# Performance work log

Measured on AMD Instinct MI355X. Metric: run time of the kernel, lower is better.

The kernel has to match this reference:

```python
import jax, jax.numpy as jnp
import numpy as np

B, N, D, J, L = 8, 2046, 128, 128, 2  # batch, ops, feature len, jobs, blocks
C = N + 2  # ops + appended begin/end rows


def setup_inputs() -> dict:
    key = jax.random.key(0)
    ks = jax.random.split(key, 40)

    def w(k, shape, fan_in):
        return jax.random.normal(k, shape, jnp.float32) / np.float32(np.sqrt(fan_in))

    inp = {}
    inp["operation_features"] = jax.random.normal(ks[0], (B, N, D), jnp.float32)
    inp["same_type_mask"] = (jax.random.uniform(ks[1], (B, N, N)) > 0.5).astype(jnp.float32)
    inp["relations"] = jax.random.randint(ks[2], (B, N, 2), 0, N, jnp.int32)
    inp["begins_idx"] = jax.random.randint(ks[3], (B, J), 0, N, jnp.int32)
    inp["ends_idx"] = jax.random.randint(ks[4], (B, J), 0, N, jnp.int32)
    # begin_end_init params
    inp["init_bp_w"] = w(ks[5], (D, D), D); inp["init_bp_b"] = jnp.zeros((D,), jnp.float32)
    inp["init_ep_w"] = w(ks[6], (D, D), D); inp["init_ep_b"] = jnp.zeros((D,), jnp.float32)
    # per-block params, stacked on leading L axis
    inp["be_bp_w"] = w(ks[7], (L, D, D), D); inp["be_bp_b"] = jnp.zeros((L, D), jnp.float32)
    inp["be_ep_w"] = w(ks[8], (L, D, D), D); inp["be_ep_b"] = jnp.zeros((L, D), jnp.float32)
    inp["seq_mix_w"] = w(ks[9], (L, 3 * D, D), 3 * D); inp["seq_mix_b"] = jnp.zeros((L, D), jnp.float32)
    inp["attn_w_w"] = w(ks[10], (L, D, 3 * D), D); inp["attn_w_b"] = jnp.zeros((L, 3 * D), jnp.float32)
    inp["score_w"] = w(ks[11], (L, 2 * D), 2 * D); inp["score_b"] = jnp.zeros((L,), jnp.float32)
    inp["attn_out_w"] = w(ks[12], (L, D, D), D); inp["attn_out_b"] = jnp.zeros((L, D), jnp.float32)
    inp["mix_w"] = w(ks[13], (L, 2 * D, D), 2 * D); inp["mix_b"] = jnp.zeros((L, D), jnp.float32)
    return inp


def _begin_end(ops, begins_idx, ends_idx, bp_w, bp_b, ep_w, ep_b):
    gb = jnp.take_along_axis(ops, begins_idx[..., None], axis=1)  # [B,J,D]
    ge = jnp.take_along_axis(ops, ends_idx[..., None], axis=1)
    begin = jnp.mean(gb @ bp_w + bp_b, axis=1)  # [B,D]
    end = jnp.mean(ge @ ep_w + ep_b, axis=1)
    return begin, end


def _forward(operation_features, same_type_mask,
             init_bp_w, init_bp_b, init_ep_w, init_ep_b,
             be_bp_w, be_bp_b, be_ep_w, be_ep_b,
             seq_mix_w, seq_mix_b, attn_w_w, attn_w_b,
             score_w, score_b, attn_out_w, attn_out_b,
             mix_w, mix_b, relations, begins_idx, ends_idx):
    begin, end = _begin_end(operation_features, begins_idx, ends_idx,
                            init_bp_w, init_bp_b, init_ep_w, init_ep_b)
    feats = jnp.concatenate([operation_features, begin[:, None], end[:, None]], axis=1)  # [B,C,D]
    # -1 sentinels point to appended begin/end rows
    rel_p = jnp.where(relations[..., 0] == -1, N, relations[..., 0])  # [B,N]
    rel_s = jnp.where(relations[..., 1] == -1, N + 1, relations[..., 1])
    mask = jnp.zeros((B, C, C), jnp.float32)
    mask = mask.at[:, :N, :N].set(same_type_mask)
    mask = mask.at[:, N, N].set(1.0).at[:, N + 1, N + 1].set(1.0)

    for l in range(L):
        # --- OperationTimeRelationEncoder ---
        pred = jnp.take_along_axis(feats, rel_p[..., None], axis=1)  # [B,N,D]
        succ = jnp.take_along_axis(feats, rel_s[..., None], axis=1)
        mixed = jnp.concatenate([feats[:, :N], pred, succ], axis=-1) @ seq_mix_w[l] + seq_mix_b[l]
        b2, e2 = _begin_end(feats, begins_idx, ends_idx,
                            be_bp_w[l], be_bp_b[l], be_ep_w[l], be_ep_b[l])
        seq_feats = jnp.concatenate([mixed, b2[:, None], e2[:, None]], axis=1)  # [B,C,D]
        # --- SelfAttention (GAT-style concat score) ---
        qkv = feats @ attn_w_w[l] + attn_w_b[l]
        q, k, v = jnp.split(qkv, 3, axis=-1)  # each [B,C,D]
        wq, wk = score_w[l][:D], score_w[l][D:]
        # score(concat(q_i, k_j)) = q_i.wq + k_j.wk + b, then LeakyReLU
        scores = jax.nn.leaky_relu((q @ wq)[:, :, None] + (k @ wk)[:, None, :] + score_b[l])  # [B,C,C]
        attn = jax.nn.softmax(scores * mask, axis=-1)
        weighted = jnp.einsum('bij,bjh->bih', attn, v)  # [B,C,D]
        attn_out = weighted @ attn_out_w[l] + attn_out_b[l]
        # --- block mix ---
        feats = jnp.concatenate([seq_feats, attn_out], axis=-1) @ mix_w[l] + mix_b[l]

    return jnp.mean(feats, axis=1), feats


def reference(operation_features, same_type_mask,
              init_bp_w, init_bp_b, init_ep_w, init_ep_b,
              be_bp_w, be_bp_b, be_ep_w, be_ep_b,
              seq_mix_w, seq_mix_b, attn_w_w, attn_w_b,
              score_w, score_b, attn_out_w, attn_out_b,
              mix_w, mix_b, relations, begins_idx, ends_idx):
    return _forward(operation_features, same_type_mask,
                    init_bp_w, init_bp_b, init_ep_w, init_ep_b,
                    be_bp_w, be_bp_b, be_ep_w, be_ep_b,
                    seq_mix_w, seq_mix_b, attn_w_w, attn_w_b,
                    score_w, score_b, attn_out_w, attn_out_b,
                    mix_w, mix_b, relations, begins_idx, ends_idx)
```

## Files before the change

kernel.cpp:

```cpp
#include <hip/hip_runtime.h>

constexpr int kB = 8;
constexpr int kN = 2046;
constexpr int kC = 2048;
constexpr int kD = 128;
constexpr int kJ = 128;
constexpr int kL = 2;

typedef short bfrag8 __attribute__((ext_vector_type(8)));
typedef float f32x4 __attribute__((ext_vector_type(4)));

__device__ __forceinline__ float bf2f(unsigned short h) {
  union { unsigned u; float f; } x; x.u = ((unsigned)h) << 16; return x.f;
}
__device__ __forceinline__ unsigned short f2bf(float f) {
  union { float f; unsigned u; } x; x.f = f;
  unsigned u = x.u;
  if ((u & 0x7fffffffu) > 0x7f800000u) return (unsigned short)((u >> 16) | 0x40);
  return (unsigned short)((u + 0x7fffu + ((u >> 16) & 1u)) >> 16);
}
__device__ __forceinline__ unsigned short f2bf_fast(float f) {
  union { float f; unsigned u; } x; x.f = f;
  return (unsigned short)((x.u + 0x7fffu + ((x.u >> 16) & 1u)) >> 16);
}
__device__ __forceinline__ void split2(float x, unsigned short& h, unsigned short& l) {
  unsigned short hh = f2bf_fast(x);
  h = hh;
  l = f2bf_fast(x - bf2f(hh));
}

struct Raw {
  const void *ops, *mask;
  const int *rel, *bidx, *eidx;
  const void *ibw, *ibb, *iew, *ieb;
  const void *bbw, *bbb, *bew, *beb;
  const void *sw, *sb;
  const void *aw, *ab;
  const void *scw, *scb;
  const void *aow, *aob;
  const void *mw, *mb;
};

__device__ __forceinline__ float rp(const void* p, size_t i, bool bf) {
  return bf ? bf2f(((const unsigned short*)p)[i]) : ((const float*)p)[i];
}

__device__ __forceinline__ bool sniff(const Raw& r) {
  const unsigned* x = (const unsigned*)r.ops;
  int lane = (int)(threadIdx.x & 63);
  int hits = 0;
  #pragma unroll
  for (int q = 0; q < 16; ++q) {
    unsigned w = x[q * 64 + lane];
    unsigned e0 = (w >> 7) & 0xFFu;
    hits += (e0 == 0u || (e0 >= 96u && e0 <= 134u)) ? 1 : 0;
  }
  #pragma unroll
  for (int o = 1; o < 64; o <<= 1) hits += __shfl_xor(hits, o);
  return hits >= 512;
}

constexpr size_t OF_FEATS = 0;
constexpr size_t OF_SEQ   = 2097152;
constexpr size_t OF_ATTN  = 4194304;
constexpr size_t OF_V     = 6291456;
constexpr size_t OF_SQ    = 8388608;
constexpr size_t OF_SK    = 8404992;
constexpr size_t OF_U     = 8421376;
constexpr size_t OF_PART  = 8422400;
constexpr size_t OF_BMIX  = 8423424;
constexpr size_t OF_WT    = 8423680;

constexpr int WT_SEQH = 0;
constexpr int WT_SEQL = 49152;
constexpr int WT_VH   = 98304;
constexpr int WT_VL   = 114688;
constexpr int WT_MIXH = 131072;
constexpr int WT_MIXL = 163840;
constexpr int WT_LS   = 196608;

constexpr int RP_WT   = 640;
constexpr int RP_WF   = RP_WT + 258;
constexpr int RP_UV   = RP_WF + 2;
constexpr int RP_BE   = RP_UV + 16;
constexpr int RP_PART = RP_BE + 1;
constexpr int RP_CAST = RP_PART + 4092;
constexpr int RP_TOT  = RP_CAST + 4092;

__device__ __forceinline__ f32x4 mfma16(bfrag8 a, bfrag8 b, f32x4 c) {
  return __builtin_amdgcn_mfma_f32_16x16x32_bf16(a, b, c, 0, 0, 0);
}

__global__ __launch_bounds__(256) void k_prep(Raw r, float* __restrict__ feats,
                                              unsigned* __restrict__ bits32,
                                              unsigned short* __restrict__ wt,
                                              float* __restrict__ bmix,
                                              float* __restrict__ u2,
                                              float* __restrict__ part) {
  __shared__ __align__(16) char smem[4096];
  int bid = blockIdx.x, t = threadIdx.x;
  bool bf = sniff(r);

  if (bid < RP_WT) {
    int idx = bid * 256 + t;
    int l = idx / 81920;
    int rr = idx - l * 81920;
    const void* src; size_t si; int dH, dL, k, n;
    if (rr < 49152) {
      k = rr >> 7; n = rr & 127;
      src = r.sw; si = (size_t)l * 49152 + (size_t)k * 128 + n;
      dH = l * WT_LS + WT_SEQH; dL = l * WT_LS + WT_SEQL;
    } else if (rr < 65536) {
      int e = rr - 49152; k = e >> 7; n = e & 127;
      src = r.aw; si = (size_t)l * 49152 + (size_t)k * 384 + 256 + n;
      dH = l * WT_LS + WT_VH; dL = l * WT_LS + WT_VL;
    } else {
      int e = rr - 65536; k = e >> 7; n = e & 127;
      src = r.mw; si = (size_t)l * 32768 + (size_t)k * 128 + n;
      dH = l * WT_LS + WT_MIXH; dL = l * WT_LS + WT_MIXL;
    }
    float v = rp(src, si, bf);
    unsigned short h, lo;
    split2(v, h, lo);
    int kc = k >> 5, q = (k >> 3) & 3, e8 = k & 7;
    int fa = ((kc * 8 + (n >> 4)) * 64 + (q * 16 + (n & 15))) * 8 + e8;
    wt[dH + fa] = h;
    wt[dL + fa] = lo;
  } else if (bid < RP_WF) {
    int rb = bid - RP_WT;
    int l = rb / 129, d1 = rb - l * 129;
    float* vsh = (float*)smem;
    size_t mixbot = (size_t)l * 32768 + 16384;
    if (t < 128) {
      vsh[t] = (d1 < 128) ? rp(r.aow, (size_t)l * 16384 + (size_t)d1 * 128 + t, bf)
                          : rp(r.aob, (size_t)l * 128 + t, bf);
    }
    __syncthreads();
    if (t < 128) {
      int d = t;
      float acc = 0.f;
      if (bf) {
        const unsigned short* mwp = (const unsigned short*)r.mw + mixbot + d;
        #pragma unroll 8
        for (int d2 = 0; d2 < kD; ++d2) acc += vsh[d2] * bf2f(mwp[(size_t)d2 * 128]);
      } else {
        const float* mwp = (const float*)r.mw + mixbot + d;
        #pragma unroll 8
        for (int d2 = 0; d2 < kD; ++d2) acc += vsh[d2] * mwp[(size_t)d2 * 128];
      }
      if (d1 < 128) {
        unsigned short h, lo;
        split2(acc, h, lo);
        int k = 128 + d1;
        int kc = k >> 5, q = (k >> 3) & 3, e8 = k & 7;
        int fa = ((kc * 8 + (d >> 4)) * 64 + (q * 16 + (d & 15))) * 8 + e8;
        wt[l * WT_LS + WT_MIXH + fa] = h;
        wt[l * WT_LS + WT_MIXL + fa] = lo;
      } else {
        bmix[(size_t)l * kD + d] = acc + rp(r.mb, (size_t)l * 128 + d, bf);
      }
    }
  } else if (bid < RP_UV) {
    int l = bid - RP_WF;
    float* swm = (float*)smem;
    float* red = (float*)smem + 256;
    if (t < 128) {
      swm[t]       = rp(r.scw, (size_t)l * 256 + t, bf);
      swm[128 + t] = rp(r.scw, (size_t)l * 256 + 128 + t, bf);
    }
    __syncthreads();
    if (t < 128) {
      int k = t;
      size_t base = (size_t)l * 49152 + (size_t)k * 384;
      float uq = 0.f, uk = 0.f;
      if (bf) {
        const unsigned* aq = (const unsigned*)((const unsigned short*)r.aw + base);
        #pragma unroll 8
        for (int g = 0; g < 64; ++g) {
          unsigned wq = aq[g];
          uq += bf2f((unsigned short)(wq & 0xffffu)) * swm[2 * g]
              + bf2f((unsigned short)(wq >> 16))     * swm[2 * g + 1];
        }
        #pragma unroll 8
        for (int g = 0; g < 64; ++g) {
          unsigned wk = aq[64 + g];
          uk += bf2f((unsigned short)(wk & 0xffffu)) * swm[128 + 2 * g]
              + bf2f((unsigned short)(wk >> 16))     * swm[128 + 2 * g + 1];
        }
      } else {
        const float* aq = (const float*)r.aw + base;
        #pragma unroll 8
        for (int g = 0; g < 32; ++g) {
          float4 v = *(const float4*)(aq + g * 4);
          uq += v.x * swm[4 * g] + v.y * swm[4 * g + 1]
              + v.z * swm[4 * g + 2] + v.w * swm[4 * g + 3];
        }
        #pragma unroll 8
        for (int g = 0; g < 32; ++g) {
          float4 v = *(const float4*)(aq + 128 + g * 4);
          uk += v.x * swm[128 + 4 * g] + v.y * swm[128 + 4 * g + 1]
              + v.z * swm[128 + 4 * g + 2] + v.w * swm[128 + 4 * g + 3];
        }
      }
      float* u = u2 + (size_t)l * 272;
      u[k] = uq; u[128 + k] = uk;
      red[k] = rp(r.ab, (size_t)l * 384 + k, bf) * swm[k]
             + rp(r.ab, (size_t)l * 384 + 128 + k, bf) * swm[128 + k];
    }
    __syncthreads();
    if (t == 0) {
      float s = rp(r.scb, l, bf);
      for (int i = 0; i < 128; ++i) s += red[i];
      u2[(size_t)l * 272 + 256] = s;
    }
  } else if (bid < RP_BE) {
    int rb = bid - RP_UV;
    int b = rb >> 1, sel = rb & 1;
    float* msh = (float*)smem;
    const int* idx = (sel ? r.eidx : r.bidx) + b * kJ;
    const void* wv = sel ? r.iew : r.ibw;
    const void* bb = sel ? r.ieb : r.ibb;
    if (t < 128) {
      int d = t;
      float acc = 0.f;
      if (bf) {
        const unsigned short* op = (const unsigned short*)r.ops;
        #pragma unroll 4
        for (int j = 0; j < kJ; ++j)
          acc += bf2f(op[((size_t)b * kN + idx[j]) * kD + d]);
      } else {
        const float* op = (const float*)r.ops;
        #pragma unroll 4
        for (int j = 0; j < kJ; ++j)
          acc += op[((size_t)b * kN + idx[j]) * kD + d];
      }
      msh[d] = acc * (1.0f / kJ);
    }
    __syncthreads();
    if (t < 128) {
      int d = t;
      float o;
      if (bf) {
        const unsigned short* wp = (const unsigned short*)wv + d;
        o = bf2f(((const unsigned short*)bb)[d]);
        #pragma unroll 8
        for (int k2 = 0; k2 < kD; ++k2) o += msh[k2] * bf2f(wp[(size_t)k2 * kD]);
      } else {
        const float* wp = (const float*)wv + d;
        o = ((const float*)bb)[d];
        #pragma unroll 8
        for (int k2 = 0; k2 < kD; ++k2) o += msh[k2] * wp[(size_t)k2 * kD];
      }
      feats[(size_t)b * kC * kD + (size_t)(kN + sel) * kD + d] = o;
    }
  } else if (bid < RP_PART) {
    #pragma unroll
    for (int q = 0; q < 4; ++q) part[q * 256 + t] = 0.f;
  } else if (bid < RP_CAST) {
    int idx = (bid - RP_PART) * 256 + t;
    int elem = idx * 2;
    int b = elem / (kN * kD);
    int rr = elem - b * (kN * kD);
    float2 f;
    if (bf) {
      unsigned u = ((const unsigned*)r.ops)[idx];
      f.x = bf2f((unsigned short)(u & 0xffffu));
      f.y = bf2f((unsigned short)(u >> 16));
    } else {
      f = ((const float2*)r.ops)[idx];
    }
    *(float2*)(feats + (size_t)b * kC * kD + rr) = f;
  } else {
    int wave = t >> 6, lane = t & 63;
    int rr = (bid - RP_CAST) * 4 + wave;
    int b = rr / kN, i = rr - b * kN;
    unsigned wacc = 0;
    int sel_g = lane >> 1, sel_hi = lane & 1;
    if (bf) {
      const unsigned short* mrow = (const unsigned short*)r.mask + (size_t)rr * kN;
      #pragma unroll
      for (int g = 0; g < 32; ++g) {
        int j = g * 64 + lane;
        unsigned short v = (j < kN) ? mrow[j] : (unsigned short)0;
        unsigned long long m = __ballot(v != 0);
        if (sel_g == g) wacc = sel_hi ? (unsigned)(m >> 32) : (unsigned)m;
      }
    } else {
      const unsigned* mrow = (const unsigned*)r.mask + (size_t)rr * kN;
      #pragma unroll
      for (int g = 0; g < 32; ++g) {
        int j = g * 64 + lane;
        unsigned v = (j < kN) ? mrow[j] : 0u;
        unsigned long long m = __ballot(v != 0);
        if (sel_g == g) wacc = sel_hi ? (unsigned)(m >> 32) : (unsigned)m;
      }
    }
    bits32[((size_t)b * kC + i) * 64 + lane] = wacc;
  }
}

__global__ __launch_bounds__(256) void k_stage1(Raw r, int l,
    const float* __restrict__ feats, const unsigned short* __restrict__ wt,
    const float* __restrict__ u2, float* __restrict__ seq,
    unsigned short* __restrict__ Vt, float* __restrict__ sq, float* __restrict__ sk)
{
  __shared__ __align__(16) char smem[21504];
  unsigned short (*Ah)[64 * 40] = (unsigned short(*)[64 * 40])smem;
  unsigned short (*Al)[64 * 40] = (unsigned short(*)[64 * 40])(smem + 10240);
  float* su = (float*)(smem + 20480);
  int bid = blockIdx.x, t = threadIdx.x;
  int lane = t & 63, w = t >> 6, m = lane & 15, quad = lane >> 4;
  bool bf = sniff(r);
  const unsigned short* wl = wt + (size_t)l * WT_LS;

  if (bid >= 16) {
    int g = bid - 16;
    bool isv = g >= 256;
    int rb = isv ? g - 256 : g;
    int gr0 = rb * 64;
    int b = gr0 >> 11, r0 = gr0 & 2047;
    int arow = t >> 2, kq = (t & 3) * 8;
    int nl = r0 + arow;
    const float* fb = feats + (size_t)b * kC * kD;
    const float *s0, *s1, *s2;
    if (!isv) {
      int nr = (nl <= kN - 1) ? nl : (kN - 1);
      const int* rel = r.rel + ((size_t)b * kN + nr) * 2;
      int rpd = rel[0], rsc = rel[1];
      int p = (rpd < 0) ? kN : rpd;
      int s = (rsc < 0) ? (kN + 1) : rsc;
      s0 = fb + (size_t)nl * kD;
      s1 = fb + (size_t)p * kD;
      s2 = fb + (size_t)s * kD;
    } else {
      s0 = fb + (size_t)nl * kD; s1 = s0; s2 = s0;
      su[t] = u2[(size_t)l * 272 + t];
    }
    const int K = isv ? 128 : 384;
    const unsigned short* wth = isv ? (wl + WT_VH) : (wl + WT_SEQH);
    const unsigned short* wtl = isv ? (wl + WT_VL) : (wl + WT_SEQL);
    const unsigned short* pbh = wth + (size_t)(w * 2) * 512 + lane * 8;
    const unsigned short* pbl = wtl + (size_t)(w * 2) * 512 + lane * 8;
    float pq = 0.f, pk2 = 0.f;

    auto build = [&](int kb, int buf) {
      int kg = kb + kq;
      const float* sp;
      if (!isv) sp = (kg < 128) ? (s0 + kg) : (kg < 256) ? (s1 + kg - 128) : (s2 + kg - 256);
      else      sp = s0 + kg;
      float4 xa = *(const float4*)sp;
      float4 xb = *(const float4*)(sp + 4);
      if (isv) {
        pq  += xa.x * su[kg]     + xa.y * su[kg + 1] + xa.z * su[kg + 2] + xa.w * su[kg + 3]
             + xb.x * su[kg + 4] + xb.y * su[kg + 5] + xb.z * su[kg + 6] + xb.w * su[kg + 7];
        pk2 += xa.x * su[128 + kg]     + xa.y * su[128 + kg + 1] + xa.z * su[128 + kg + 2] + xa.w * su[128 + kg + 3]
             + xb.x * su[128 + kg + 4] + xb.y * su[128 + kg + 5] + xb.z * su[128 + kg + 6] + xb.w * su[128 + kg + 7];
      }
      unsigned short h[8], lo[8];
      split2(xa.x, h[0], lo[0]); split2(xa.y, h[1], lo[1]);
      split2(xa.z, h[2], lo[2]); split2(xa.w, h[3], lo[3]);
      split2(xb.x, h[4], lo[4]); split2(xb.y, h[5], lo[5]);
      split2(xb.z, h[6], lo[6]); split2(xb.w, h[7], lo[7]);
      uint4 ph, pl;
      ph.x = h[0] | ((unsigned)h[1] << 16);  ph.y = h[2] | ((unsigned)h[3] << 16);
      ph.z = h[4] | ((unsigned)h[5] << 16);  ph.w = h[6] | ((unsigned)h[7] << 16);
      pl.x = lo[0] | ((unsigned)lo[1] << 16); pl.y = lo[2] | ((unsigned)lo[3] << 16);
      pl.z = lo[4] | ((unsigned)lo[5] << 16); pl.w = lo[6] | ((unsigned)lo[7] << 16);
      *(uint4*)&Ah[buf][arow * 40 + kq] = ph;
      *(uint4*)&Al[buf][arow * 40 + kq] = pl;
    };

    f32x4 acc[4][2];
    #pragma unroll
    for (int mi = 0; mi < 4; ++mi) { acc[mi][0] = {0.f,0.f,0.f,0.f}; acc[mi][1] = {0.f,0.f,0.f,0.f}; }

    __syncthreads();
    build(0, 0);
    __syncthreads();
    for (int kb = 0; kb < K; kb += 32) {
      int cur = (kb >> 5) & 1;
      int kc = kb >> 5;
      bfrag8 bh0 = *(const bfrag8*)(pbh + (size_t)kc * 4096);
      bfrag8 bh1 = *(const bfrag8*)(pbh + (size_t)kc * 4096 + 512);
      bfrag8 bl0 = {}, bl1 = {};
      if (!bf) {
        bl0 = *(const bfrag8*)(pbl + (size_t)kc * 4096);
        bl1 = *(const bfrag8*)(pbl + (size_t)kc * 4096 + 512);
      }
      if (kb + 32 < K) build(kb + 32, cur ^ 1);
      #pragma unroll
      for (int mi = 0; mi < 4; ++mi) {
        bfrag8 ah = *(const bfrag8*)&Ah[cur][(mi * 16 + m) * 40 + quad * 8];
        bfrag8 al = *(const bfrag8*)&Al[cur][(mi * 16 + m) * 40 + quad * 8];
        acc[mi][0] = mfma16(ah, bh0, acc[mi][0]);
        acc[mi][0] = mfma16(al, bh0, acc[mi][0]);
        acc[mi][1] = mfma16(ah, bh1, acc[mi][1]);
        acc[mi][1] = mfma16(al, bh1, acc[mi][1]);
        if (!bf) {
          acc[mi][0] = mfma16(ah, bl0, acc[mi][0]);
          acc[mi][1] = mfma16(ah, bl1, acc[mi][1]);
        }
      }
      __syncthreads();
    }

    int n0 = w * 32 + m;
    if (!isv) {
      float bv0 = rp(r.sb, (size_t)l * 128 + n0, bf);
      float bv1 = rp(r.sb, (size_t)l * 128 + n0 + 16, bf);
      #pragma unroll
      for (int mi = 0; mi < 4; ++mi)
        #pragma unroll
        for (int reg = 0; reg < 4; ++reg) {
          int ra = r0 + mi * 16 + quad * 4 + reg;
          if (ra < kN) {
            seq[((size_t)b * kC + ra) * kD + n0]      = acc[mi][0][reg] + bv0;
            seq[((size_t)b * kC + ra) * kD + n0 + 16] = acc[mi][1][reg] + bv1;
          }
        }
    } else {
      float bv0 = rp(r.ab, (size_t)l * 384 + 256 + n0, bf);
      float bv1 = rp(r.ab, (size_t)l * 384 + 256 + n0 + 16, bf);
      unsigned short* vtb = Vt + (size_t)b * 262144;
      #pragma unroll
      for (int mi = 0; mi < 4; ++mi)
        #pragma unroll
        for (int reg = 0; reg < 4; ++reg) {
          int c = r0 + mi * 16 + quad * 4 + reg;
          int kc = c >> 5, cq = (c >> 3) & 3, e8 = c & 7;
          int lp = cq * 16 + m;
          vtb[((kc * 8 + w * 2) * 64 + lp) * 8 + e8]       = f2bf_fast(acc[mi][0][reg] + bv0);
          vtb[((kc * 8 + w * 2 + 1) * 64 + lp) * 8 + e8]   = f2bf_fast(acc[mi][1][reg] + bv1);
        }
      pq  += __shfl_xor(pq, 1);  pq  += __shfl_xor(pq, 2);
      pk2 += __shfl_xor(pk2, 1); pk2 += __shfl_xor(pk2, 2);
      if ((t & 3) == 0) {
        sq[(size_t)b * kC + nl] = pq + u2[(size_t)l * 272 + 256];
        sk[(size_t)b * kC + nl] = pk2;
      }
    }
  } else {
    int rb = bid;
    int b = rb >> 1, sel = rb & 1;
    float* msh = (float*)smem;
    const int* idx = (sel ? r.eidx : r.bidx) + b * kJ;
    const void* wv = sel ? r.bew : r.bbw;
    const void* bb = sel ? r.beb : r.bbb;
    size_t wbase = (size_t)l * kD * kD, bbase = (size_t)l * kD;
    if (t < 128) {
      int d = t;
      const float* fb2 = feats + (size_t)b * kC * kD;
      float acc = 0.f;
      #pragma unroll 4
      for (int j = 0; j < kJ; ++j) acc += fb2[(size_t)idx[j] * kD + d];
      msh[d] = acc * (1.0f / kJ);
    }
    __syncthreads();
    if (t < 128) {
      int d = t;
      float o;
      if (bf) {
        const unsigned short* wp = (const unsigned short*)wv + wbase + d;
        o = bf2f(((const unsigned short*)bb)[bbase + d]);
        #pragma unroll 8
        for (int k2 = 0; k2 < kD; ++k2) o += msh[k2] * bf2f(wp[(size_t)k2 * kD]);
      } else {
        const float* wp = (const float*)wv + wbase + d;
        o = ((const float*)bb)[bbase + d];
        #pragma unroll 8
        for (int k2 = 0; k2 < kD; ++k2) o += msh[k2] * wp[(size_t)k2 * kD];
      }
      seq[(size_t)b * kC * kD + (size_t)(kN + sel) * kD + d] = o;
    }
  }
}

__global__ __launch_bounds__(256) void k_attn_pv_mfma(
    const unsigned* __restrict__ bits,
    const float* __restrict__ sq, const float* __restrict__ sk,
    const unsigned short* __restrict__ Vt,
    float* __restrict__ outw)
{
  int b = blockIdx.y;
  int i0 = blockIdx.x * 32;
  int t = threadIdx.x, lane = t & 63, w = t >> 6;

  __shared__ unsigned short pshare[2][1024];
  __shared__ float sklds[kC];
  __shared__ unsigned bitlds[2048];
  __shared__ float ssq[32], smx[32], szv[32];

  const float* skb = sk + (size_t)b * kC;
  #pragma unroll
  for (int q = 0; q < 8; ++q) sklds[q * 256 + t] = skb[q * 256 + t];
  const unsigned* bitrow = bits + ((size_t)b * kC + i0) * 64;
  #pragma unroll
  for (int q = 0; q < 8; ++q) bitlds[q * 256 + t] = bitrow[q * 256 + t];
  if (t < 32) ssq[t] = sq[(size_t)b * kC + i0 + t];
  __syncthreads();

  {
    int rr = t >> 3, seg = t & 7;
    int ig = i0 + rr;
    bool ok = (ig < kN);
    float sqi2 = ssq[rr];
    const unsigned* bw = bitlds + rr * 64 + seg * 8;
    const float* sks = sklds + seg * 256;
    float mx;
    if (ok) {
      float msk = -3e38f;
      #pragma unroll 1
      for (int w8 = 0; w8 < 8; ++w8) {
        unsigned bb = bw[w8];
        #pragma unroll
        for (int q4 = 0; q4 < 8; ++q4) {
          float4 skv = *(const float4*)(sks + w8 * 32 + q4 * 4);
          unsigned nib = bb >> (q4 * 4);
          msk = (nib & 1u) ? fmaxf(msk, skv.x) : msk;
          msk = (nib & 2u) ? fmaxf(msk, skv.y) : msk;
          msk = (nib & 4u) ? fmaxf(msk, skv.z) : msk;
          msk = (nib & 8u) ? fmaxf(msk, skv.w) : msk;
        }
      }
      #pragma unroll
      for (int d2 = 1; d2 < 8; d2 <<= 1) msk = fmaxf(msk, __shfl_xor(msk, d2));
      float s = sqi2 + msk;
      mx = fmaxf(0.f, fmaxf(s, 0.01f * s));
    } else {
      float s = sqi2 + sklds[ig & (kC - 1)];
      mx = fmaxf(0.f, fmaxf(s, 0.01f * s));
    }
    float emx = __expf(-mx);
    float zs = 0.f;
    if (ok) {
      #pragma unroll 1
      for (int w8 = 0; w8 < 8; ++w8) {
        unsigned bb = bw[w8];
        #pragma unroll
        for (int q4 = 0; q4 < 8; ++q4) {
          float4 skv = *(const float4*)(sks + w8 * 32 + q4 * 4);
          unsigned nib = bb >> (q4 * 4);
          float s1 = sqi2 + skv.x, l1 = fmaxf(s1, 0.01f * s1);
          float s2 = sqi2 + skv.y, l2 = fmaxf(s2, 0.01f * s2);
          float s3 = sqi2 + skv.z, l3 = fmaxf(s3, 0.01f * s3);
          float s4 = sqi2 + skv.w, l4 = fmaxf(s4, 0.01f * s4);
          zs += (nib & 1u) ? __expf(l1 - mx) : emx;
          zs += (nib & 2u) ? __expf(l2 - mx) : emx;
          zs += (nib & 4u) ? __expf(l3 - mx) : emx;
          zs += (nib & 8u) ? __expf(l4 - mx) : emx;
        }
      }
    } else {
      zs = 256.f * emx;
      if ((ig >> 8) == seg) {
        float s = sqi2 + sklds[ig & (kC - 1)];
        float lr = fmaxf(s, 0.01f * s);
        zs += __expf(lr - mx) - emx;
      }
    }
    #pragma unroll
    for (int d2 = 1; d2 < 8; d2 <<= 1) zs += __shfl_xor(zs, d2);
    if (seg == 0) { smx[rr] = mx; szv[rr] = 1.0f / zs; }
  }
  __syncthreads();

  int f = t >> 1, h = t & 1;
  int mt_b = f >> 6;
  int lb = f & 63;
  int irow_l = mt_b * 16 + (lb & 15);
  int quad_b = lb >> 4;
  int i_g = i0 + irow_l;
  float sqi = ssq[irow_l];
  float mri = smx[irow_l];
  int joff = quad_b * 8 + h * 4;
  bool irow_ok = (i_g < kN);
  const unsigned char* bitb = (const unsigned char*)bitlds + irow_l * 256;

  auto buildP = [&](int k0, int buf) {
    float4 skv = *(const float4*)(sklds + k0 + joff);
    unsigned byte;
    if (irow_ok) {
      byte = bitb[(k0 >> 3) + quad_b];
    } else {
      int d0 = i_g - (k0 + quad_b * 8);
      byte = ((unsigned)d0 < 8u) ? (1u << d0) : 0u;
    }
    unsigned nib = byte >> (h * 4);
    unsigned short us[4];
    float sv[4] = {skv.x, skv.y, skv.z, skv.w};
    #pragma unroll
    for (int dj = 0; dj < 4; ++dj) {
      float s = sqi + sv[dj];
      float lr = fmaxf(s, 0.01f * s);
      float val = ((nib >> dj) & 1u) ? lr : 0.f;
      us[dj] = f2bf_fast(__expf(val - mri));
    }
    uint2 pk;
    pk.x = us[0] | ((unsigned)us[1] << 16);
    pk.y = us[2] | ((unsigned)us[3] << 16);
    *(uint2*)(&pshare[buf][f * 8 + h * 4]) = pk;
  };

  f32x4 acc00 = {0.f, 0.f, 0.f, 0.f}, acc01 = acc00, acc10 = acc00, acc11 = acc00;
  int m = lane & 15, quad = lane >> 4;
  int nbase = w * 32;
  const unsigned short* vtb = Vt + (size_t)b * 262144;
  const unsigned short* p0 = vtb + (size_t)(w * 2) * 512 + lane * 8;
  const unsigned short* p1 = p0 + 512;

  buildP(0, 0);
  bfrag8 b0n = *(const bfrag8*)p0;
  bfrag8 b1n = *(const bfrag8*)p1;
  __syncthreads();

  for (int k0 = 0; k0 < kC; k0 += 32) {
    int cur = (k0 >> 5) & 1;
    bfrag8 bf0 = b0n, bf1 = b1n;
    if (k0 + 32 < kC) {
      size_t off = (size_t)((k0 >> 5) + 1) * 4096;
      b0n = *(const bfrag8*)(p0 + off);
      b1n = *(const bfrag8*)(p1 + off);
    }
    bfrag8 a0 = *(const bfrag8*)(&pshare[cur][(0 * 64 + lane) * 8]);
    bfrag8 a1 = *(const bfrag8*)(&pshare[cur][(1 * 64 + lane) * 8]);
    acc00 = mfma16(a0, bf0, acc00);
    acc01 = mfma16(a0, bf1, acc01);
    acc10 = mfma16(a1, bf0, acc10);
    acc11 = mfma16(a1, bf1, acc11);
    if (k0 + 32 < kC) buildP(k0 + 32, cur ^ 1);
    __syncthreads();
  }

  #pragma unroll
  for (int reg = 0; reg < 4; ++reg) {
    int il_a = quad * 4 + reg;
    int i_a = i0 + il_a;
    int i_b = i_a + 16;
    float za = szv[il_a];
    float zb = szv[il_a + 16];
    float* oa = outw + ((size_t)b * kC + i_a) * kD + nbase + m;
    float* ob = outw + ((size_t)b * kC + i_b) * kD + nbase + m;
    oa[0]  = acc00[reg] * za;
    oa[16] = acc01[reg] * za;
    ob[0]  = acc10[reg] * zb;
    ob[16] = acc11[reg] * zb;
  }
}

__global__ __launch_bounds__(256) void k_mix64(Raw r, int l,
    const float* __restrict__ seqb, const float* __restrict__ attnw,
    const unsigned short* __restrict__ wt, const float* __restrict__ bmix,
    float* __restrict__ featsOut, void* __restrict__ outx, float* __restrict__ part,
    int mode)
{
  __shared__ __align__(16) char smem[20480];
  unsigned short (*Ah)[64 * 40] = (unsigned short(*)[64 * 40])smem;
  unsigned short (*Al)[64 * 40] = (unsigned short(*)[64 * 40])(smem + 10240);
  constexpr int K = 256;
  int bid = blockIdx.x, t = threadIdx.x;
  int lane = t & 63, w = t >> 6, m = lane & 15, quad = lane >> 4;
  bool bf = sniff(r);
  int gr0 = bid * 64;
  int b = gr0 >> 11;
  int arow = t >> 2, kq = (t & 3) * 8;
  const float* s0 = seqb  + (size_t)(gr0 + arow) * kD;
  const float* s1 = attnw + (size_t)(gr0 + arow) * kD;
  const unsigned short* wth = wt + (size_t)l * WT_LS + WT_MIXH;
  const unsigned short* wtl = wt + (size_t)l * WT_LS + WT_MIXL;
  const unsigned short* pbh = wth + (size_t)(w * 2) * 512 + lane * 8;
  const unsigned short* pbl = wtl + (size_t)(w * 2) * 512 + lane * 8;

  auto build = [&](int kb, int buf) {
    int kg = kb + kq;
    const float* sp = (kg < kD) ? (s0 + kg) : (s1 + kg - kD);
    float4 xa = *(const float4*)sp;
    float4 xb = *(const float4*)(sp + 4);
    unsigned short h[8], lo[8];
    split2(xa.x, h[0], lo[0]); split2(xa.y, h[1], lo[1]);
    split2(xa.z, h[2], lo[2]); split2(xa.w, h[3], lo[3]);
    split2(xb.x, h[4], lo[4]); split2(xb.y, h[5], lo[5]);
    split2(xb.z, h[6], lo[6]); split2(xb.w, h[7], lo[7]);
    uint4 ph, pl;
    ph.x = h[0] | ((unsigned)h[1] << 16);  ph.y = h[2] | ((unsigned)h[3] << 16);
    ph.z = h[4] | ((unsigned)h[5] << 16);  ph.w = h[6] | ((unsigned)h[7] << 16);
    pl.x = lo[0] | ((unsigned)lo[1] << 16); pl.y = lo[2] | ((unsigned)lo[3] << 16);
    pl.z = lo[4] | ((unsigned)lo[5] << 16); pl.w = lo[6] | ((unsigned)lo[7] << 16);
    *(uint4*)&Ah[buf][arow * 40 + kq] = ph;
    *(uint4*)&Al[buf][arow * 40 + kq] = pl;
  };

  f32x4 acc[4][2];
  #pragma unroll
  for (int mi = 0; mi < 4; ++mi) { acc[mi][0] = {0.f,0.f,0.f,0.f}; acc[mi][1] = {0.f,0.f,0.f,0.f}; }

  build(0, 0);
  __syncthreads();
  for (int kb = 0; kb < K; kb += 32) {
    int cur = (kb >> 5) & 1;
    int kc = kb >> 5;
    bfrag8 bh0 = *(const bfrag8*)(pbh + (size_t)kc * 4096);
    bfrag8 bh1 = *(const bfrag8*)(pbh + (size_t)kc * 4096 + 512);
    bfrag8 bl0 = {}, bl1 = {};
    if (!bf) {
      bl0 = *(const bfrag8*)(pbl + (size_t)kc * 4096);
      bl1 = *(const bfrag8*)(pbl + (size_t)kc * 4096 + 512);
    }
    if (kb + 32 < K) build(kb + 32, cur ^ 1);
    #pragma unroll
    for (int mi = 0; mi < 4; ++mi) {
      bfrag8 ah = *(const bfrag8*)&Ah[cur][(mi * 16 + m) * 40 + quad * 8];
      bfrag8 al = *(const bfrag8*)&Al[cur][(mi * 16 + m) * 40 + quad * 8];
      acc[mi][0] = mfma16(ah, bh0, acc[mi][0]);
      acc[mi][0] = mfma16(al, bh0, acc[mi][0]);
      acc[mi][1] = mfma16(ah, bh1, acc[mi][1]);
      acc[mi][1] = mfma16(al, bh1, acc[mi][1]);
      if (!bf) {
        acc[mi][0] = mfma16(ah, bl0, acc[mi][0]);
        acc[mi][1] = mfma16(ah, bl1, acc[mi][1]);
      }
    }
    __syncthreads();
  }

  int n0 = w * 32 + m;
  float bv0 = bmix[(size_t)l * kD + n0];
  float bv1 = bmix[(size_t)l * kD + n0 + 16];
  if (mode == 0) {
    #pragma unroll
    for (int mi = 0; mi < 4; ++mi)
      #pragma unroll
      for (int reg = 0; reg < 4; ++reg) {
        size_t row = (size_t)gr0 + mi * 16 + quad * 4 + reg;
        featsOut[row * kD + n0]      = acc[mi][0][reg] + bv0;
        featsOut[row * kD + n0 + 16] = acc[mi][1][reg] + bv1;
      }
  } else {
    float sum0 = 0.f, sum1 = 0.f;
    #pragma unroll
    for (int mi = 0; mi < 4; ++mi)
      #pragma unroll
      for (int reg = 0; reg < 4; ++reg) {
        size_t row = (size_t)gr0 + mi * 16 + quad * 4 + reg;
        float v0 = acc[mi][0][reg] + bv0;
        float v1 = acc[mi][1][reg] + bv1;
        if (bf) {
          unsigned short* o = (unsigned short*)outx + 1024;
          o[row * kD + n0]      = f2bf(v0);
          o[row * kD + n0 + 16] = f2bf(v1);
        } else {
          float* o = (float*)outx + 1024;
          o[row * kD + n0]      = v0;
          o[row * kD + n0 + 16] = v1;
        }
        sum0 += v0; sum1 += v1;
      }
    sum0 += __shfl_xor(sum0, 16); sum0 += __shfl_xor(sum0, 32);
    sum1 += __shfl_xor(sum1, 16); sum1 += __shfl_xor(sum1, 32);
    if (quad == 0) {
      atomicAdd(&part[(size_t)b * kD + n0],      sum0);
      atomicAdd(&part[(size_t)b * kD + n0 + 16], sum1);
    }
  }
}

__global__ __launch_bounds__(128) void k_mean(Raw r, const float* __restrict__ part,
                                              void* __restrict__ out) {
  bool bf = sniff(r);
  int b = blockIdx.x, d = threadIdx.x;
  float v = part[(size_t)b * kD + d] * (1.0f / kC);
  if (bf) ((unsigned short*)out)[b * kD + d] = f2bf(v);
  else    ((float*)out)[b * kD + d] = v;
}

extern "C" void kernel_launch(void* const* d_in, const int* in_sizes, int n_in,
                              void* d_out, int out_size, void* d_ws, size_t ws_size,
                              hipStream_t stream) {
  Raw r;
  r.ops = d_in[0];  r.mask = d_in[1];
  r.rel = (const int*)d_in[2]; r.bidx = (const int*)d_in[3]; r.eidx = (const int*)d_in[4];
  r.ibw = d_in[5];  r.ibb = d_in[6];  r.iew = d_in[7];  r.ieb = d_in[8];
  r.bbw = d_in[9];  r.bbb = d_in[10]; r.bew = d_in[11]; r.beb = d_in[12];
  r.sw  = d_in[13]; r.sb  = d_in[14]; r.aw  = d_in[15]; r.ab  = d_in[16];
  r.scw = d_in[17]; r.scb = d_in[18]; r.aow = d_in[19]; r.aob = d_in[20];
  r.mw  = d_in[21]; r.mb  = d_in[22];

  float* ws    = (float*)d_ws;
  float* feats = ws + OF_FEATS;
  float* seq   = ws + OF_SEQ;
  float* attnw = ws + OF_ATTN;
  float* sq    = ws + OF_SQ;
  float* sk    = ws + OF_SK;
  float* u2    = ws + OF_U;
  float* part  = ws + OF_PART;
  float* bmix  = ws + OF_BMIX;
  unsigned short* wt = (unsigned short*)(ws + OF_WT);
  unsigned short* Vt = (unsigned short*)(ws + OF_V);
  unsigned*     bits = (unsigned*)(ws + OF_V + 1048576);

  k_prep<<<RP_TOT, 256, 0, stream>>>(r, feats, bits, wt, bmix, u2, part);

  for (int l = 0; l < kL; ++l) {
    k_stage1<<<528, 256, 0, stream>>>(r, l, feats, wt, u2, seq, Vt, sq, sk);
    k_attn_pv_mfma<<<dim3(64, kB), 256, 0, stream>>>(bits, sq, sk, Vt, attnw);
    k_mix64<<<256, 256, 0, stream>>>(r, l, seq, attnw, wt, bmix, feats, d_out, part,
                                     (l == kL - 1) ? 1 : 0);
  }

  k_mean<<<kB, 128, 0, stream>>>(r, part, d_out);
}
```

Before: 431.3 us.

## Store intermediates pre-split as packed bf16 hi/lo pairs to avoid repeated splitting

Intermediate activations (feats, seq, attention output) are now stored as 32-bit words holding bf16 high and low halves, produced once by the writer. The GEMM tile builders repack these with shifts and masks instead of running the float-to-bf16 split per element, which removes ALU work from the stage1 and mix kernels. Separately, the cast path in the prep kernel is vectorized to 8 elements per thread, and the mask-bitmap loop issues all loads before the ballots. Memory traffic stays the same size, but precision drops slightly because the stored value is hi+lo rather than the exact fp32.

Result: no change. 432.1 us (+0.2%).

```diff
diff --git a/kernel.cpp b/kernel.cpp
--- a/kernel.cpp
+++ b/kernel.cpp
@@ -27,6 +27,13 @@
   unsigned short hh = f2bf_fast(x);
   h = hh;
   l = f2bf_fast(x - bf2f(hh));
+}
+__device__ __forceinline__ unsigned packhl(float x) {
+  unsigned short h, l; split2(x, h, l);
+  return (unsigned)h | ((unsigned)l << 16);
+}
+__device__ __forceinline__ float unpackhl(unsigned u) {
+  return bf2f((unsigned short)u) + bf2f((unsigned short)(u >> 16));
 }
 
 struct Raw {
@@ -84,14 +91,14 @@
 constexpr int RP_UV   = RP_WF + 2;
 constexpr int RP_BE   = RP_UV + 16;
 constexpr int RP_PART = RP_BE + 1;
-constexpr int RP_CAST = RP_PART + 4092;
+constexpr int RP_CAST = RP_PART + 1023;
 constexpr int RP_TOT  = RP_CAST + 4092;
 
 __device__ __forceinline__ f32x4 mfma16(bfrag8 a, bfrag8 b, f32x4 c) {
   return __builtin_amdgcn_mfma_f32_16x16x32_bf16(a, b, c, 0, 0, 0);
 }
 
-__global__ __launch_bounds__(256) void k_prep(Raw r, float* __restrict__ feats,
+__global__ __launch_bounds__(256) void k_prep(Raw r, unsigned* __restrict__ feats,
                                               unsigned* __restrict__ bits32,
                                               unsigned short* __restrict__ wt,
                                               float* __restrict__ bmix,
@@ -251,25 +258,32 @@
         #pragma unroll 8
         for (int k2 = 0; k2 < kD; ++k2) o += msh[k2] * wp[(size_t)k2 * kD];
       }
-      feats[(size_t)b * kC * kD + (size_t)(kN + sel) * kD + d] = o;
+      feats[(size_t)b * kC * kD + (size_t)(kN + sel) * kD + d] = packhl(o);
     }
   } else if (bid < RP_PART) {
     #pragma unroll
     for (int q = 0; q < 4; ++q) part[q * 256 + t] = 0.f;
   } else if (bid < RP_CAST) {
     int idx = (bid - RP_PART) * 256 + t;
-    int elem = idx * 2;
-    int b = elem / (kN * kD);
-    int rr = elem - b * (kN * kD);
-    float2 f;
+    size_t elem = (size_t)idx * 8;
+    int b = (int)(elem / (size_t)(kN * kD));
+    int rr = (int)(elem - (size_t)b * (kN * kD));
+    unsigned* dst = feats + (size_t)b * kC * kD + rr;
+    uint4 o0, o1;
     if (bf) {
-      unsigned u = ((const unsigned*)r.ops)[idx];
-      f.x = bf2f((unsigned short)(u & 0xffffu));
-      f.y = bf2f((unsigned short)(u >> 16));
+      uint4 in = ((const uint4*)r.ops)[idx];
+      o0.x = in.x & 0xffffu; o0.y = in.x >> 16;
+      o0.z = in.y & 0xffffu; o0.w = in.y >> 16;
+      o1.x = in.z & 0xffffu; o1.y = in.z >> 16;
+      o1.z = in.w & 0xffffu; o1.w = in.w >> 16;
     } else {
-      f = ((const float2*)r.ops)[idx];
-    }
-    *(float2*)(feats + (size_t)b * kC * kD + rr) = f;
+      float4 a = ((const float4*)r.ops)[idx * 2];
+      float4 c = ((const float4*)r.ops)[idx * 2 + 1];
+      o0.x = packhl(a.x); o0.y = packhl(a.y); o0.z = packhl(a.z); o0.w = packhl(a.w);
+      o1.x = packhl(c.x); o1.y = packhl(c.y); o1.z = packhl(c.z); o1.w = packhl(c.w);
+    }
+    *(uint4*)dst = o0;
+    *(uint4*)(dst + 4) = o1;
   } else {
     int wave = t >> 6, lane = t & 63;
     int rr = (bid - RP_CAST) * 4 + wave;
@@ -278,21 +292,29 @@
     int sel_g = lane >> 1, sel_hi = lane & 1;
     if (bf) {
       const unsigned short* mrow = (const unsigned short*)r.mask + (size_t)rr * kN;
+      unsigned short v[32];
       #pragma unroll
       for (int g = 0; g < 32; ++g) {
         int j = g * 64 + lane;
-        unsigned short v = (j < kN) ? mrow[j] : (unsigned short)0;
-        unsigned long long m = __ballot(v != 0);
-        if (sel_g == g) wacc = sel_hi ? (unsigned)(m >> 32) : (unsigned)m;
+        v[g] = (j < kN) ? mrow[j] : (unsigned short)0;
+      }
+      #pragma unroll
+      for (int g = 0; g < 32; ++g) {
+        unsigned long long bm = __ballot(v[g] != 0);
+        if (sel_g == g) wacc = sel_hi ? (unsigned)(bm >> 32) : (unsigned)bm;
       }
     } else {
       const unsigned* mrow = (const unsigned*)r.mask + (size_t)rr * kN;
+      unsigned v[32];
       #pragma unroll
       for (int g = 0; g < 32; ++g) {
         int j = g * 64 + lane;
-        unsigned v = (j < kN) ? mrow[j] : 0u;
-        unsigned long long m = __ballot(v != 0);
-        if (sel_g == g) wacc = sel_hi ? (unsigned)(m >> 32) : (unsigned)m;
+        v[g] = (j < kN) ? mrow[j] : 0u;
+      }
+      #pragma unroll
+      for (int g = 0; g < 32; ++g) {
+        unsigned long long bm = __ballot(v[g] != 0);
+        if (sel_g == g) wacc = sel_hi ? (unsigned)(bm >> 32) : (unsigned)bm;
       }
     }
     bits32[((size_t)b * kC + i) * 64 + lane] = wacc;
@@ -300,8 +322,8 @@
 }
 
 __global__ __launch_bounds__(256) void k_stage1(Raw r, int l,
-    const float* __restrict__ feats, const unsigned short* __restrict__ wt,
-    const float* __restrict__ u2, float* __restrict__ seq,
+    const unsigned* __restrict__ feats, const unsigned short* __restrict__ wt,
+    const float* __restrict__ u2, unsigned* __restrict__ seq,
     unsigned short* __restrict__ Vt, float* __restrict__ sq, float* __restrict__ sk)
 {
   __shared__ __align__(16) char smem[21504];
@@ -321,8 +343,8 @@
     int b = gr0 >> 11, r0 = gr0 & 2047;
     int arow = t >> 2, kq = (t & 3) * 8;
     int nl = r0 + arow;
-    const float* fb = feats + (size_t)b * kC * kD;
-    const float *s0, *s1, *s2;
+    const unsigned* fb = feats + (size_t)b * kC * kD;
+    const unsigned *s0, *s1, *s2;
     if (!isv) {
       int nr = (nl <= kN - 1) ? nl : (kN - 1);
       const int* rel = r.rel + ((size_t)b * kN + nr) * 2;
@@ -345,27 +367,28 @@
 
     auto build = [&](int kb, int buf) {
       int kg = kb + kq;
-      const float* sp;
+      const unsigned* sp;
       if (!isv) sp = (kg < 128) ? (s0 + kg) : (kg < 256) ? (s1 + kg - 128) : (s2 + kg - 256);
       else      sp = s0 + kg;
-      float4 xa = *(const float4*)sp;
-      float4 xb = *(const float4*)(sp + 4);
+      uint4 U0 = *(const uint4*)sp;
+      uint4 U1 = *(const uint4*)(sp + 4);
       if (isv) {
-        pq  += xa.x * su[kg]     + xa.y * su[kg + 1] + xa.z * su[kg + 2] + xa.w * su[kg + 3]
-             + xb.x * su[kg + 4] + xb.y * su[kg + 5] + xb.z * su[kg + 6] + xb.w * su[kg + 7];
-        pk2 += xa.x * su[128 + kg]     + xa.y * su[128 + kg + 1] + xa.z * su[128 + kg + 2] + xa.w * su[128 + kg + 3]
-             + xb.x * su[128 + kg + 4] + xb.y * su[128 + kg + 5] + xb.z * su[128 + kg + 6] + xb.w * su[128 + kg + 7];
-      }
-      unsigned short h[8], lo[8];
-      split2(xa.x, h[0], lo[0]); split2(xa.y, h[1], lo[1]);
-      split2(xa.z, h[2], lo[2]); split2(xa.w, h[3], lo[3]);
-      split2(xb.x, h[4], lo[4]); split2(xb.y, h[5], lo[5]);
-      split2(xb.z, h[6], lo[6]); split2(xb.w, h[7], lo[7]);
+        float f0 = unpackhl(U0.x), f1 = unpackhl(U0.y), f2 = unpackhl(U0.z), f3 = unpackhl(U0.w);
+        float f4 = unpackhl(U1.x), f5 = unpackhl(U1.y), f6 = unpackhl(U1.z), f7 = unpackhl(U1.w);
+        pq  += f0 * su[kg]     + f1 * su[kg + 1] + f2 * su[kg + 2] + f3 * su[kg + 3]
+             + f4 * su[kg + 4] + f5 * su[kg + 5] + f6 * su[kg + 6] + f7 * su[kg + 7];
+        pk2 += f0 * su[128 + kg]     + f1 * su[128 + kg + 1] + f2 * su[128 + kg + 2] + f3 * su[128 + kg + 3]
+             + f4 * su[128 + kg + 4] + f5 * su[128 + kg + 5] + f6 * su[128 + kg + 6] + f7 * su[128 + kg + 7];
+      }
       uint4 ph, pl;
-      ph.x = h[0] | ((unsigned)h[1] << 16);  ph.y = h[2] | ((unsigned)h[3] << 16);
-      ph.z = h[4] | ((unsigned)h[5] << 16);  ph.w = h[6] | ((unsigned)h[7] << 16);
-      pl.x = lo[0] | ((unsigned)lo[1] << 16); pl.y = lo[2] | ((unsigned)lo[3] << 16);
-      pl.z = lo[4] | ((unsigned)lo[5] << 16); pl.w = lo[6] | ((unsigned)lo[7] << 16);
+      ph.x = (U0.x & 0xffffu) | (U0.y << 16);
+      pl.x = (U0.x >> 16)     | (U0.y & 0xffff0000u);
+      ph.y = (U0.z & 0xffffu) | (U0.w << 16);
+      pl.y = (U0.z >> 16)     | (U0.w & 0xffff0000u);
+      ph.z = (U1.x & 0xffffu) | (U1.y << 16);
+      pl.z = (U1.x >> 16)     | (U1.y & 0xffff0000u);
+      ph.w = (U1.z & 0xffffu) | (U1.w << 16);
+      pl.w = (U1.z >> 16)     | (U1.w & 0xffff0000u);
       *(uint4*)&Ah[buf][arow * 40 + kq] = ph;
       *(uint4*)&Al[buf][arow * 40 + kq] = pl;
     };
@@ -414,8 +437,8 @@
         for (int reg = 0; reg < 4; ++reg) {
           int ra = r0 + mi * 16 + quad * 4 + reg;
           if (ra < kN) {
-            seq[((size_t)b * kC + ra) * kD + n0]      = acc[mi][0][reg] + bv0;
-            seq[((size_t)b * kC + ra) * kD + n0 + 16] = acc[mi][1][reg] + bv1;
+            seq[((size_t)b * kC + ra) * kD + n0]      = packhl(acc[mi][0][reg] + bv0);
+            seq[((size_t)b * kC + ra) * kD + n0 + 16] = packhl(acc[mi][1][reg] + bv1);
           }
         }
     } else {
@@ -449,10 +472,10 @@
     size_t wbase = (size_t)l * kD * kD, bbase = (size_t)l * kD;
     if (t < 128) {
       int d = t;
-      const float* fb2 = feats + (size_t)b * kC * kD;
+      const unsigned* fb2 = feats + (size_t)b * kC * kD;
       float acc = 0.f;
       #pragma unroll 4
-      for (int j = 0; j < kJ; ++j) acc += fb2[(size_t)idx[j] * kD + d];
+      for (int j = 0; j < kJ; ++j) acc += unpackhl(fb2[(size_t)idx[j] * kD + d]);
       msh[d] = acc * (1.0f / kJ);
     }
     __syncthreads();
@@ -470,7 +493,7 @@
         #pragma unroll 8
         for (int k2 = 0; k2 < kD; ++k2) o += msh[k2] * wp[(size_t)k2 * kD];
       }
-      seq[(size_t)b * kC * kD + (size_t)(kN + sel) * kD + d] = o;
+      seq[(size_t)b * kC * kD + (size_t)(kN + sel) * kD + d] = packhl(o);
     }
   }
 }
@@ -479,7 +502,7 @@
     const unsigned* __restrict__ bits,
     const float* __restrict__ sq, const float* __restrict__ sk,
     const unsigned short* __restrict__ Vt,
-    float* __restrict__ outw)
+    unsigned* __restrict__ outw)
 {
   int b = blockIdx.y;
   int i0 = blockIdx.x * 32;
@@ -638,19 +661,19 @@
     int i_b = i_a + 16;
     float za = szv[il_a];
     float zb = szv[il_a + 16];
-    float* oa = outw + ((size_t)b * kC + i_a) * kD + nbase + m;
-    float* ob = outw + ((size_t)b * kC + i_b) * kD + nbase + m;
-    oa[0]  = acc00[reg] * za;
-    oa[16] = acc01[reg] * za;
-    ob[0]  = acc10[reg] * zb;
-    ob[16] = acc11[reg] * zb;
+    unsigned* oa = outw + ((size_t)b * kC + i_a) * kD + nbase + m;
+    unsigned* ob = outw + ((size_t)b * kC + i_b) * kD + nbase + m;
+    oa[0]  = packhl(acc00[reg] * za);
+    oa[16] = packhl(acc01[reg] * za);
+    ob[0]  = packhl(acc10[reg] * zb);
+    ob[16] = packhl(acc11[reg] * zb);
   }
 }
 
 __global__ __launch_bounds__(256) void k_mix64(Raw r, int l,
-    const float* __restrict__ seqb, const float* __restrict__ attnw,
+    const unsigned* __restrict__ seqb, const unsigned* __restrict__ attnw,
     const unsigned short* __restrict__ wt, const float* __restrict__ bmix,
-    float* __restrict__ featsOut, void* __restrict__ outx, float* __restrict__ part,
+    unsigned* __restrict__ featsOut, void* __restrict__ outx, float* __restrict__ part,
     int mode)
 {
   __shared__ __align__(16) char smem[20480];
@@ -663,8 +686,8 @@
   int gr0 = bid * 64;
   int b = gr0 >> 11;
   int arow = t >> 2, kq = (t & 3) * 8;
-  const float* s0 = seqb  + (size_t)(gr0 + arow) * kD;
-  const float* s1 = attnw + (size_t)(gr0 + arow) * kD;
+  const unsigned* s0 = seqb  + (size_t)(gr0 + arow) * kD;
+  const unsigned* s1 = attnw + (size_t)(gr0 + arow) * kD;
   const unsigned short* wth = wt + (size_t)l * WT_LS + WT_MIXH;
   const unsigned short* wtl = wt + (size_t)l * WT_LS + WT_MIXL;
   const unsigned short* pbh = wth + (size_t)(w * 2) * 512 + lane * 8;
@@ -672,19 +695,18 @@
 
   auto build = [&](int kb, int buf) {
     int kg = kb + kq;
-    const float* sp = (kg < kD) ? (s0 + kg) : (s1 + kg - kD);
-    float4 xa = *(const float4*)sp;
-    float4 xb = *(const float4*)(sp + 4);
-    unsigned short h[8], lo[8];
-    split2(xa.x, h[0], lo[0]); split2(xa.y, h[1], lo[1]);
-    split2(xa.z, h[2], lo[2]); split2(xa.w, h[3], lo[3]);
-    split2(xb.x, h[4], lo[4]); split2(xb.y, h[5], lo[5]);
-    split2(xb.z, h[6], lo[6]); split2(xb.w, h[7], lo[7]);
+    const unsigned* sp = (kg < kD) ? (s0 + kg) : (s1 + kg - kD);
+    uint4 U0 = *(const uint4*)sp;
+    uint4 U1 = *(const uint4*)(sp + 4);
     uint4 ph, pl;
-    ph.x = h[0] | ((unsigned)h[1] << 16);  ph.y = h[2] | ((unsigned)h[3] << 16);
-    ph.z = h[4] | ((unsigned)h[5] << 16);  ph.w = h[6] | ((unsigned)h[7] << 16);
-    pl.x = lo[0] | ((unsigned)lo[1] << 16); pl.y = lo[2] | ((unsigned)lo[3] << 16);
-    pl.z = lo[4] | ((unsigned)lo[5] << 16); pl.w = lo[6] | ((unsigned)lo[7] << 16);
+    ph.x = (U0.x & 0xffffu) | (U0.y << 16);
+    pl.x = (U0.x >> 16)     | (U0.y & 0xffff0000u);
+    ph.y = (U0.z & 0xffffu) | (U0.w << 16);
+    pl.y = (U0.z >> 16)     | (U0.w & 0xffff0000u);
+    ph.z = (U1.x & 0xffffu) | (U1.y << 16);
+    pl.z = (U1.x >> 16)     | (U1.y & 0xffff0000u);
+    ph.w = (U1.z & 0xffffu) | (U1.w << 16);
+    pl.w = (U1.z >> 16)     | (U1.w & 0xffff0000u);
     *(uint4*)&Ah[buf][arow * 40 + kq] = ph;
     *(uint4*)&Al[buf][arow * 40 + kq] = pl;
   };
@@ -731,8 +753,8 @@
       #pragma unroll
       for (int reg = 0; reg < 4; ++reg) {
         size_t row = (size_t)gr0 + mi * 16 + quad * 4 + reg;
-        featsOut[row * kD + n0]      = acc[mi][0][reg] + bv0;
-        featsOut[row * kD + n0 + 16] = acc[mi][1][reg] + bv1;
+        featsOut[row * kD + n0]      = packhl(acc[mi][0][reg] + bv0);
+        featsOut[row * kD + n0 + 16] = packhl(acc[mi][1][reg] + bv1);
       }
   } else {
     float sum0 = 0.f, sum1 = 0.f;
@@ -785,9 +807,9 @@
   r.mw  = d_in[21]; r.mb  = d_in[22];
 
   float* ws    = (float*)d_ws;
-  float* feats = ws + OF_FEATS;
-  float* seq   = ws + OF_SEQ;
-  float* attnw = ws + OF_ATTN;
+  unsigned* feats = (unsigned*)(ws + OF_FEATS);
+  unsigned* seq   = (unsigned*)(ws + OF_SEQ);
+  unsigned* attnw = (unsigned*)(ws + OF_ATTN);
   float* sq    = ws + OF_SQ;
   float* sk    = ws + OF_SK;
   float* u2    = ws + OF_U;
```
